# Optimization experiments

Hardware: AMD Instinct MI355X
Metric: run time of the kernel (lower is better)

Reference implementation:

```python
import jax, jax.numpy as jnp
import numpy as np

EMBED = 1024
HEADS = 16
HDIM = 64
OUT = 1024
SCALE = HDIM ** (-0.5)


def setup_inputs() -> dict:
    key = jax.random.key(0)
    ks = jax.random.split(key, 12)
    B, L = 4, 1024
    k = jax.random.normal(ks[0], (B, L, EMBED), dtype=jnp.float32)
    q = jax.random.normal(ks[1], (B, L, EMBED), dtype=jnp.float32)
    v = jax.random.normal(ks[2], (B, L, EMBED), dtype=jnp.float32)
    # Linear params stored as [in, out]; scaled like torch default init
    lim = EMBED ** (-0.5)
    Wq = jax.random.uniform(ks[3], (EMBED, HEADS * HDIM), jnp.float32, -lim, lim)
    bq = jax.random.uniform(ks[4], (HEADS * HDIM,), jnp.float32, -lim, lim)
    Wk = jax.random.uniform(ks[5], (EMBED, HEADS * HDIM), jnp.float32, -lim, lim)
    Wv = jax.random.uniform(ks[6], (EMBED, HEADS * HDIM), jnp.float32, -lim, lim)
    limp = (HEADS * HDIM) ** (-0.5)
    Wp = jax.random.uniform(ks[7], (HEADS * HDIM, OUT), jnp.float32, -limp, limp)
    bp = jax.random.uniform(ks[8], (OUT,), jnp.float32, -limp, limp)
    attn_w = jax.random.uniform(ks[9], (2 * HDIM,), jnp.float32, -SCALE, SCALE)
    gamma = jnp.ones((OUT,), jnp.float32)
    beta = jnp.zeros((OUT,), jnp.float32)
    return {"k": k, "q": q, "v": v, "Wq": Wq, "bq": bq, "Wk": Wk, "Wv": Wv,
            "Wp": Wp, "bp": bp, "attn_w": attn_w, "gamma": gamma, "beta": beta}


def reference(k, q, v, Wq, bq, Wk, Wv, Wp, bp, attn_w, gamma, beta):
    B, Lq = q.shape[0], q.shape[1]
    Lk = k.shape[1]
    # QKV projections -> (b, len, heads, hdim)
    qh = (q @ Wq + bq).reshape(B, Lq, HEADS, HDIM)
    kh = (k @ Wk).reshape(B, Lk, HEADS, HDIM)
    vh = (v @ Wv).reshape(B, Lk, HEADS, HDIM)
    # mlp score: tanh(cat(q_i, k_j) . w) == tanh(q_i.w1 + k_j.w2); avoids
    # materializing the (b, q, k, n, 2d) padded tensor from the original.
    w1, w2 = attn_w[:HDIM], attn_w[HDIM:]
    sq = jnp.einsum('bind,d->bin', qh, w1)  # (b, q_len, heads)
    sk = jnp.einsum('bjnd,d->bjn', kh, w2)  # (b, k_len, heads)
    attn = jnp.tanh(sq[:, :, None, :] + sk[:, None, :, :])  # (b, i, j, n)
    attn = jax.nn.softmax(attn, axis=2)  # softmax over k_len (dim=2)
    out = jnp.einsum('bijn,bjnd->bind', attn, vh).reshape(B, Lq, HEADS * HDIM)
    out = out @ Wp + bp
    # LayerNorm eps=1e-6 (dropout is identity at p=0)
    mean = jnp.mean(out, axis=-1, keepdims=True)
    var = jnp.var(out, axis=-1, keepdims=True)
    out = (out - mean) / jnp.sqrt(var + 1e-6) * gamma + beta
    return out
```

## Files before the change

kernel.cpp:

```cpp
#include <hip/hip_runtime.h>
#include <math.h>

#define HEADS 16
#define HDIM  64
#define SEQ   1024
#define ROWS  4096
#define EMB   1024
#define MN    16

typedef _Float16 f16;
typedef __attribute__((ext_vector_type(4))) _Float16 f16x4;
typedef __attribute__((ext_vector_type(8))) _Float16 f16x8;
typedef __attribute__((ext_vector_type(4))) float f32x4;

__global__ __launch_bounds__(256) void fold_kernel(
    const float* __restrict__ Wq, const float* __restrict__ Wk,
    const float* __restrict__ bq, const float* __restrict__ attn_w,
    float* __restrict__ uq, float* __restrict__ uk, float* __restrict__ cq)
{
  int bid = blockIdx.x;
  if (bid < 128) {
    int idx = bid*256 + threadIdx.x;
    bool isQ = idx < 16384;
    int li = isQ ? idx : idx - 16384;
    int e = li >> 4, n = li & 15;
    const float* W = isQ ? Wq : Wk;
    const float* w = isQ ? attn_w : attn_w + HDIM;
    const float* wp = &W[(size_t)e*EMB + n*HDIM];
    float s = 0.f;
    #pragma unroll 16
    for (int d = 0; d < HDIM; ++d) s = fmaf(wp[d], w[d], s);
    (isQ ? uq : uk)[li] = s;
  } else if (threadIdx.x < 16) {
    int n = threadIdx.x;
    float s = 0.f;
    for (int d = 0; d < HDIM; ++d) s = fmaf(bq[n*HDIM+d], attn_w[d], s);
    cq[n] = s;
  }
}

__global__ __launch_bounds__(256) void sqsk2_kernel(
    const float* __restrict__ q, const float* __restrict__ k,
    const float* __restrict__ uq, const float* __restrict__ uk,
    const float* __restrict__ cq, float* __restrict__ sq, float* __restrict__ sk)
{
  __shared__ float rowbuf[8][EMB];
  __shared__ float part[16][8][17];
  int bid = blockIdx.x;
  bool isQ = bid < 512;
  int row0 = (isQ ? bid : bid - 512) * 8;
  const float* X = isQ ? q : k;
  const float* U = isQ ? uq : uk;
  int tid = threadIdx.x;
  #pragma unroll
  for (int p = 0; p < 8; ++p) {
    int fi = p*256 + tid;
    int r = fi >> 8, c4 = (fi & 255) * 4;
    *reinterpret_cast<float4*>(&rowbuf[r][c4]) =
        *reinterpret_cast<const float4*>(&X[(size_t)(row0 + r)*EMB + c4]);
  }
  __syncthreads();
  int n = tid & 15, ch = tid >> 4;
  float acc[8] = {0,0,0,0,0,0,0,0};
  #pragma unroll 4
  for (int e0 = 0; e0 < 64; ++e0) {
    int e = ch*64 + e0;
    float u = U[e*16 + n];
    #pragma unroll
    for (int r = 0; r < 8; ++r) acc[r] = fmaf(rowbuf[r][e], u, acc[r]);
  }
  #pragma unroll
  for (int r = 0; r < 8; ++r) part[ch][r][n] = acc[r];
  __syncthreads();
  if (tid < 128) {
    int r = tid >> 4, nn = tid & 15;
    float t = isQ ? cq[nn] : 0.f;
    #pragma unroll
    for (int c = 0; c < 16; ++c) t += part[c][r][nn];
    (isQ ? sq : sk)[(size_t)(row0 + r)*16 + nn] = t;
  }
}

__global__ __launch_bounds__(256) void nodes_kernel(const float* __restrict__ sq,
                                                    float* __restrict__ nodes)
{
  int bn = blockIdx.x;
  int b = bn >> 4, n = bn & 15;
  int tid = threadIdx.x;
  float mn = 1e30f, mx = -1e30f;
  #pragma unroll
  for (int s = 0; s < 4; ++s) {
    float v = sq[((size_t)(b*SEQ + tid + s*256))*16 + n];
    mn = fminf(mn, v); mx = fmaxf(mx, v);
  }
  __shared__ float smn[256], smx[256];
  smn[tid] = mn; smx[tid] = mx;
  __syncthreads();
  for (int off = 128; off > 0; off >>= 1) {
    if (tid < off) { smn[tid] = fminf(smn[tid], smn[tid+off]);
                     smx[tid] = fmaxf(smx[tid], smx[tid+off]); }
    __syncthreads();
  }
  if (tid < MN) {
    float c = 0.5f*(smn[0] + smx[0]);
    float r = fmaxf(0.5f*(smx[0] - smn[0]), 1e-4f);
    nodes[bn*MN + tid] = c + r * cosf(tid * (3.14159265358979323f / (MN-1)));
  }
}

__global__ __launch_bounds__(256) void wprepv_kernel(
    const float* __restrict__ Wv, f16* __restrict__ Th, f16* __restrict__ Tl)
{
  __shared__ float tile[64][65];
  int k0 = blockIdx.y * 64, n0 = blockIdx.x * 64;
  int t = threadIdx.x, rr = t >> 4, c4 = (t & 15) * 4;
  #pragma unroll
  for (int i = 0; i < 4; ++i) {
    int row = rr + i * 16;
    float4 w = *reinterpret_cast<const float4*>(&Wv[(size_t)(k0 + row) * EMB + n0 + c4]);
    tile[row][c4] = w.x; tile[row][c4+1] = w.y;
    tile[row][c4+2] = w.z; tile[row][c4+3] = w.w;
  }
  __syncthreads();
  #pragma unroll
  for (int i = 0; i < 4; ++i) {
    int nn = rr + i * 16;
    f16x4 hh, ll;
    #pragma unroll
    for (int jj = 0; jj < 4; ++jj) {
      float x = tile[c4 + jj][nn];
      f16 h = (f16)x;
      hh[jj] = h; ll[jj] = (f16)(x - (float)h);
    }
    *reinterpret_cast<f16x4*>(&Th[(size_t)(n0 + nn) * EMB + k0 + c4]) = hh;
    *reinterpret_cast<f16x4*>(&Tl[(size_t)(n0 + nn) * EMB + k0 + c4]) = ll;
  }
}

__global__ __launch_bounds__(256) void vtrans_kernel(
    const float* __restrict__ v, f16* __restrict__ Th, f16* __restrict__ Tl)
{
  __shared__ float tile[64][65];
  int b = blockIdx.z;
  int j0 = blockIdx.y * 64, e0 = blockIdx.x * 64;
  int t = threadIdx.x, rr = t >> 4, c4 = (t & 15) * 4;
  #pragma unroll
  for (int i = 0; i < 4; ++i) {
    int row = rr + i * 16;
    float4 w = *reinterpret_cast<const float4*>(
        &v[((size_t)(b*SEQ + j0 + row))*EMB + e0 + c4]);
    tile[row][c4] = w.x; tile[row][c4+1] = w.y;
    tile[row][c4+2] = w.z; tile[row][c4+3] = w.w;
  }
  __syncthreads();
  #pragma unroll
  for (int i = 0; i < 4; ++i) {
    int el = rr + i * 16;
    f16x4 hh, ll;
    #pragma unroll
    for (int jj = 0; jj < 4; ++jj) {
      float x = tile[c4 + jj][el];
      f16 h = (f16)x;
      hh[jj] = h; ll[jj] = (f16)(x - (float)h);
    }
    size_t o = ((size_t)(b*EMB + e0 + el))*SEQ + j0 + c4;
    *reinterpret_cast<f16x4*>(&Th[o]) = hh;
    *reinterpret_cast<f16x4*>(&Tl[o]) = ll;
  }
}

__global__ __launch_bounds__(256) void wmat_kernel(
    const float* __restrict__ sk, const float* __restrict__ nodes,
    f16* __restrict__ wh, f16* __restrict__ wl, float* __restrict__ Wn)
{
  __shared__ float sksh[256], nodesh[MN], Wnl[MN];
  const int qd = blockIdx.x, n = blockIdx.y, b = blockIdx.z;
  const int tid = threadIdx.x;
  const int j = qd*256 + tid;
  sksh[tid] = sk[((size_t)(b*SEQ + j))*16 + n];
  if (tid < MN) { nodesh[tid] = nodes[(b*16+n)*MN + tid]; Wnl[tid] = 0.f; }
  __syncthreads();
  const float skv = sksh[tid];
  const int lane = tid & 63;
  #pragma unroll 4
  for (int m = 0; m < MN; ++m) {
    float s = nodesh[m] + skv;
    float e2 = __expf(2.f * s);
    float th = 1.f - 2.f / (e2 + 1.f);
    float w = __expf(th);
    f16 h = (f16)w;
    size_t row = (size_t)(b*256 + n*MN + m);
    wh[row*1024 + j] = h;
    wl[row*1024 + j] = (f16)(w - (float)h);
    float ws = w;
    #pragma unroll
    for (int off = 32; off > 0; off >>= 1) ws += __shfl_xor(ws, off);
    if (lane == 0) atomicAdd(&Wnl[m], ws);
  }
  __syncthreads();
  if (tid < MN) atomicAdd(&Wn[(b*16+n)*MN + tid], Wnl[tid]);
}

__global__ __launch_bounds__(256) void gemm1_64(
    const f16* __restrict__ Ah, const f16* __restrict__ Al,
    const f16* __restrict__ Bh, const f16* __restrict__ Bl,
    f16* __restrict__ Ch, f16* __restrict__ Cl)
{
  __shared__ __align__(16) char lds[32768];
  const int tid = threadIdx.x;
  const int wid = tid >> 6, lane = tid & 63;
  int flat = blockIdx.y * 16 + blockIdx.x;
  int swz = (flat & 7) * 32 + (flat >> 3);
  const int bx = swz & 15, by = swz >> 4;
  const int z = by >> 2;
  const int grow = by * 64;
  const int bcol = bx * 64;
  const int wm = wid >> 1, wn = wid & 1;
  const int asel = lane >> 4, l15 = lane & 15;
  const int K = 1024, N = 1024;
  const f16* Bz_h = Bh + (size_t)z*EMB*SEQ;
  const f16* Bz_l = Bl + (size_t)z*EMB*SEQ;

  f32x4 acc[2][2];
  #pragma unroll
  for (int i = 0; i < 2; ++i)
    #pragma unroll
    for (int jx = 0; jx < 2; ++jx)
      acc[i][jx] = (f32x4){0.f, 0.f, 0.f, 0.f};

  for (int t = 0; t < 16; ++t) {
    const int k0 = t * 64;
    __syncthreads();
    #pragma unroll
    for (int r = 0; r < 8; ++r) {
      int ci = ((r & 1) << 8) + tid;
      int row = ci >> 3, kc = ci & 7;
      int kcg = kc ^ (row & 7);
      const f16* base = (r < 2) ? Ah : (r < 4) ? Al : (r < 6) ? Bz_h : Bz_l;
      size_t roff = (r < 4) ? (size_t)(grow + row) : (size_t)(bcol + row);
      const char* src = (const char*)(base + roff * K + k0 + kcg * 8);
      char* dst = lds + (r * 512 + ci) * 16 - (r & 1) * 4096 * 0;
      dst = lds + (r * 256 + wid * 64) * 16;
      __builtin_amdgcn_global_load_lds(
          (const __attribute__((address_space(1))) unsigned int*)src,
          (__attribute__((address_space(3))) unsigned int*)dst, 16, 0, 0);
    }
    __syncthreads();
    #pragma unroll
    for (int kk = 0; kk < 2; ++kk) {
      f16x8 afh[2], afl[2], bfh[2], bfl[2];
      #pragma unroll
      for (int mf = 0; mf < 2; ++mf) {
        int row = wm * 32 + mf * 16 + l15;
        int kcx = (kk * 4 + asel) ^ (row & 7);
        int off = row * 128 + kcx * 16;
        afh[mf] = *reinterpret_cast<const f16x8*>(lds + off);
        afl[mf] = *reinterpret_cast<const f16x8*>(lds + 8192 + off);
      }
      #pragma unroll
      for (int nf = 0; nf < 2; ++nf) {
        int col = wn * 32 + nf * 16 + l15;
        int kcx = (kk * 4 + asel) ^ (col & 7);
        int off = col * 128 + kcx * 16;
        bfh[nf] = *reinterpret_cast<const f16x8*>(lds + 16384 + off);
        bfl[nf] = *reinterpret_cast<const f16x8*>(lds + 24576 + off);
      }
      #pragma unroll
      for (int mf = 0; mf < 2; ++mf)
        #pragma unroll
        for (int nf = 0; nf < 2; ++nf) {
          acc[mf][nf] = __builtin_amdgcn_mfma_f32_16x16x32_f16(afh[mf], bfh[nf], acc[mf][nf], 0, 0, 0);
          acc[mf][nf] = __builtin_amdgcn_mfma_f32_16x16x32_f16(afh[mf], bfl[nf], acc[mf][nf], 0, 0, 0);
          acc[mf][nf] = __builtin_amdgcn_mfma_f32_16x16x32_f16(afl[mf], bfh[nf], acc[mf][nf], 0, 0, 0);
        }
    }
  }
  const int crow0 = grow + wm * 32 + asel * 4;
  const int ccol0 = bcol + wn * 32 + l15;
  #pragma unroll
  for (int nf = 0; nf < 2; ++nf)
    #pragma unroll
    for (int mf = 0; mf < 2; ++mf)
      #pragma unroll
      for (int jx = 0; jx < 4; ++jx) {
        float vv = acc[mf][nf][jx];
        f16 h = (f16)vv;
        size_t o = (size_t)(crow0 + mf*16 + jx) * N + ccol0 + nf*16;
        Ch[o] = h;
        Cl[o] = (f16)(vv - (float)h);
      }
}

__global__ __launch_bounds__(256) void gemm2_k(
    const f16* __restrict__ Ah, const f16* __restrict__ Al,
    const f16* __restrict__ Bh, const f16* __restrict__ Bl,
    const float* __restrict__ bias, float* __restrict__ Cf)
{
  __shared__ __align__(16) char lds[49152];
  const int tid = threadIdx.x;
  const int wid = tid >> 6, lane = tid & 63;
  int flat = (blockIdx.z * 8 + blockIdx.y) * 16 + blockIdx.x;
  int swz = (flat & 7) * 64 + (flat >> 3);
  const int bx = swz & 15;
  const int t2 = swz >> 4;
  const int by = t2 & 7, z = t2 >> 3;
  const int brow = by * 128;
  const int bcol = bx * 64;
  const int wm = wid >> 1, wn = wid & 1;
  const int asel = lane >> 4, l15 = lane & 15;
  const int K = 256, N = 1024, MZ = 1024;
  const f16* Az_h = Ah + (size_t)z*MZ*K;
  const f16* Az_l = Al + (size_t)z*MZ*K;
  const f16* Bz_h = Bh + (size_t)z*N*K;
  const f16* Bz_l = Bl + (size_t)z*N*K;

  f32x4 acc[4][2];
  #pragma unroll
  for (int i = 0; i < 4; ++i)
    #pragma unroll
    for (int jx = 0; jx < 2; ++jx)
      acc[i][jx] = (f32x4){0.f, 0.f, 0.f, 0.f};

  for (int t = 0; t < 4; ++t) {
    const int k0 = t * 64;
    __syncthreads();
    #pragma unroll
    for (int r = 0; r < 12; ++r) {
      const char* src;
      if (r < 8) {
        int ci = ((r & 3) << 8) + tid;
        int row = ci >> 3, kc = ci & 7;
        int kcg = kc ^ (row & 7);
        const f16* base = (r < 4) ? Az_h : Az_l;
        src = (const char*)(base + (size_t)(brow + row) * K + k0 + kcg * 8);
      } else {
        int ci = ((r & 1) << 8) + tid;
        int col = ci >> 3, kc = ci & 7;
        int kcg = kc ^ (col & 7);
        const f16* base = (r < 10) ? Bz_h : Bz_l;
        src = (const char*)(base + (size_t)(bcol + col) * K + k0 + kcg * 8);
      }
      char* dst = lds + (r * 256 + wid * 64) * 16;
      __builtin_amdgcn_global_load_lds(
          (const __attribute__((address_space(1))) unsigned int*)src,
          (__attribute__((address_space(3))) unsigned int*)dst, 16, 0, 0);
    }
    __syncthreads();
    #pragma unroll
    for (int kk = 0; kk < 2; ++kk) {
      f16x8 afh[4], afl[4], bfh[2], bfl[2];
      #pragma unroll
      for (int mf = 0; mf < 4; ++mf) {
        int row = wm * 64 + mf * 16 + l15;
        int kcx = (kk * 4 + asel) ^ (row & 7);
        int off = row * 128 + kcx * 16;
        afh[mf] = *reinterpret_cast<const f16x8*>(lds + off);
        afl[mf] = *reinterpret_cast<const f16x8*>(lds + 16384 + off);
      }
      #pragma unroll
      for (int nf = 0; nf < 2; ++nf) {
        int col = wn * 32 + nf * 16 + l15;
        int kcx = (kk * 4 + asel) ^ (col & 7);
        int off = col * 128 + kcx * 16;
        bfh[nf] = *reinterpret_cast<const f16x8*>(lds + 32768 + off);
        bfl[nf] = *reinterpret_cast<const f16x8*>(lds + 40960 + off);
      }
      #pragma unroll
      for (int mf = 0; mf < 4; ++mf)
        #pragma unroll
        for (int nf = 0; nf < 2; ++nf) {
          acc[mf][nf] = __builtin_amdgcn_mfma_f32_16x16x32_f16(afh[mf], bfh[nf], acc[mf][nf], 0, 0, 0);
          acc[mf][nf] = __builtin_amdgcn_mfma_f32_16x16x32_f16(afh[mf], bfl[nf], acc[mf][nf], 0, 0, 0);
          acc[mf][nf] = __builtin_amdgcn_mfma_f32_16x16x32_f16(afl[mf], bfh[nf], acc[mf][nf], 0, 0, 0);
        }
    }
  }
  const int crow0 = z*MZ + brow + wm * 64 + asel * 4;
  const int ccol0 = bcol + wn * 32 + l15;
  #pragma unroll
  for (int nf = 0; nf < 2; ++nf) {
    float bv = bias[ccol0 + nf * 16];
    #pragma unroll
    for (int mf = 0; mf < 4; ++mf)
      #pragma unroll
      for (int jx = 0; jx < 4; ++jx)
        Cf[(size_t)(crow0 + mf*16 + jx) * N + ccol0 + nf*16] = acc[mf][nf][jx] + bv;
  }
}

__global__ __launch_bounds__(256) void gfin_kernel(
    const f16* __restrict__ Ph, const f16* __restrict__ Pl,
    const f16* __restrict__ WvTh, const f16* __restrict__ WvTl,
    float* __restrict__ G)
{
  const int bn = blockIdx.x, n = bn & 15;
  const int w = threadIdx.x >> 6, lane = threadIdx.x & 63;
  const int l15 = lane & 15, asel = lane >> 4;
  f32x4 acc = (f32x4){0.f,0.f,0.f,0.f};
  #pragma unroll 4
  for (int ks = 0; ks < 32; ++ks) {
    size_t bo = ((size_t)(n*64 + w*16 + l15))*1024 + ks*32 + asel*8;
    f16x8 bh = *reinterpret_cast<const f16x8*>(&WvTh[bo]);
    f16x8 bl = *reinterpret_cast<const f16x8*>(&WvTl[bo]);
    size_t ao = ((size_t)(bn*MN + l15))*1024 + ks*32 + asel*8;
    f16x8 ah = *reinterpret_cast<const f16x8*>(&Ph[ao]);
    f16x8 al = *reinterpret_cast<const f16x8*>(&Pl[ao]);
    acc = __builtin_amdgcn_mfma_f32_16x16x32_f16(ah, bh, acc, 0, 0, 0);
    acc = __builtin_amdgcn_mfma_f32_16x16x32_f16(ah, bl, acc, 0, 0, 0);
    acc = __builtin_amdgcn_mfma_f32_16x16x32_f16(al, bh, acc, 0, 0, 0);
  }
  #pragma unroll
  for (int jx = 0; jx < 4; ++jx)
    G[(size_t)(bn*MN + asel*4 + jx)*64 + w*16 + l15] = acc[jx];
}

__global__ __launch_bounds__(256) void coeff2_kernel(
    const float* __restrict__ sq, const float* __restrict__ nodes,
    const float* __restrict__ Wn, f16* __restrict__ csh, f16* __restrict__ csl)
{
  __shared__ float nsh[16][MN], wsh[16][MN];
  const int ic = blockIdx.x, b = blockIdx.y;
  const int tid = threadIdx.x;
  {
    int nn = tid >> 4, mm = tid & 15;
    nsh[nn][mm] = nodes[(b*16+nn)*MN + mm];
    wsh[nn][mm] = Wn[(b*16+nn)*MN + mm];
  }
  __syncthreads();
  const int il = tid >> 4, n = tid & 15;
  const int i = ic*16 + il;
  float s = sq[((size_t)(b*SEQ + i))*16 + n];
  float lam[MN];
  float den = 0.f;
  int ex = -1;
  #pragma unroll
  for (int m = 0; m < MN; ++m) {
    float diff = s - nsh[n][m];
    float wb = ((m == 0) | (m == MN-1)) ? 0.5f : 1.0f;
    wb = (m & 1) ? -wb : wb;
    if (diff == 0.f) ex = m;
    lam[m] = wb / diff;
    den = fmaf(lam[m], wsh[n][m], den);
  }
  float rden = 1024.f / den;
  f16* hp = &csh[((size_t)(b*SEQ + i))*256 + n*MN];
  f16* lp = &csl[((size_t)(b*SEQ + i))*256 + n*MN];
  #pragma unroll
  for (int m8 = 0; m8 < 2; ++m8) {
    f16x8 hv, lv;
    #pragma unroll
    for (int jj = 0; jj < 8; ++jj) {
      int m = m8*8 + jj;
      float c = (ex >= 0) ? ((m == ex) ? 1024.f/wsh[n][ex] : 0.f) : lam[m]*rden;
      f16 h = (f16)c;
      hv[jj] = h; lv[jj] = (f16)(c - (float)h);
    }
    *reinterpret_cast<f16x8*>(&hp[m8*8]) = hv;
    *reinterpret_cast<f16x8*>(&lp[m8*8]) = lv;
  }
}

__global__ __launch_bounds__(256) void hprep_kernel(
    const float* __restrict__ G, const float* __restrict__ Wp,
    f16* __restrict__ Hsh, f16* __restrict__ Hsl)
{
  __shared__ float Gsh[MN][64];
  const int oc = blockIdx.x, n = blockIdx.y, b = blockIdx.z;
  const int bn = b*16 + n;
  const int tid = threadIdx.x;
  for (int p = tid; p < MN*64; p += 256) {
    int m = p >> 6, d = p & 63;
    Gsh[m][d] = G[(size_t)(bn*MN + m)*64 + d];
  }
  __syncthreads();
  const int o = oc*256 + tid;
  float acc[MN];
  #pragma unroll
  for (int m = 0; m < MN; ++m) acc[m] = 0.f;
  for (int d = 0; d < 64; ++d) {
    float wp = Wp[(size_t)(n*64 + d)*1024 + o];
    #pragma unroll
    for (int m = 0; m < MN; ++m) acc[m] = fmaf(wp, Gsh[m][d], acc[m]);
  }
  f16 hbuf[MN], lbuf[MN];
  #pragma unroll
  for (int m = 0; m < MN; ++m) {
    float vv = acc[m] * (1.f/1024.f);
    f16 h = (f16)vv;
    hbuf[m] = h; lbuf[m] = (f16)(vv - (float)h);
  }
  size_t base = ((size_t)(b*1024 + o))*256 + n*MN;
  #pragma unroll
  for (int m8 = 0; m8 < 2; ++m8) {
    *reinterpret_cast<f16x8*>(&Hsh[base + m8*8]) = *reinterpret_cast<f16x8*>(&hbuf[m8*8]);
    *reinterpret_cast<f16x8*>(&Hsl[base + m8*8]) = *reinterpret_cast<f16x8*>(&lbuf[m8*8]);
  }
}

__global__ __launch_bounds__(256) void ln_kernel(
    float* __restrict__ out, const float* __restrict__ gamma,
    const float* __restrict__ beta)
{
  int row = blockIdx.x, tid = threadIdx.x;
  float4 x = *reinterpret_cast<float4*>(&out[(size_t)row*EMB + tid*4]);
  float sum = x.x + x.y + x.z + x.w;
  float ssq = x.x*x.x + x.y*x.y + x.z*x.z + x.w*x.w;
  #pragma unroll
  for (int off = 32; off > 0; off >>= 1) {
    sum += __shfl_down(sum, off);
    ssq += __shfl_down(ssq, off);
  }
  __shared__ float red[8];
  int wave = tid >> 6, lane = tid & 63;
  if (lane == 0) { red[wave] = sum; red[4+wave] = ssq; }
  __syncthreads();
  if (tid == 0) {
    float a = red[0]+red[1]+red[2]+red[3];
    float qq = red[4]+red[5]+red[6]+red[7];
    float mean = a * (1.f/EMB);
    float var  = qq * (1.f/EMB) - mean*mean;
    red[0] = mean;
    red[1] = 1.0f / sqrtf(var + 1e-6f);
  }
  __syncthreads();
  float mean = red[0], inv = red[1];
  float4 gv = *reinterpret_cast<const float4*>(&gamma[tid*4]);
  float4 bv = *reinterpret_cast<const float4*>(&beta[tid*4]);
  x.x = (x.x - mean)*inv*gv.x + bv.x;
  x.y = (x.y - mean)*inv*gv.y + bv.y;
  x.z = (x.z - mean)*inv*gv.z + bv.z;
  x.w = (x.w - mean)*inv*gv.w + bv.w;
  *reinterpret_cast<float4*>(&out[(size_t)row*EMB + tid*4]) = x;
}

extern "C" void kernel_launch(void* const* d_in, const int* in_sizes, int n_in,
                              void* d_out, int out_size, void* d_ws, size_t ws_size,
                              hipStream_t stream)
{
  const float* k   = (const float*)d_in[0];
  const float* q   = (const float*)d_in[1];
  const float* v   = (const float*)d_in[2];
  const float* Wq  = (const float*)d_in[3];
  const float* bq  = (const float*)d_in[4];
  const float* Wk  = (const float*)d_in[5];
  const float* Wv  = (const float*)d_in[6];
  const float* Wp  = (const float*)d_in[7];
  const float* bp  = (const float*)d_in[8];
  const float* aw  = (const float*)d_in[9];
  const float* gamma = (const float*)d_in[10];
  const float* beta  = (const float*)d_in[11];
  float* out = (float*)d_out;

  float* ws    = (float*)d_ws;
  float* uq    = ws;
  float* uk    = uq + 16384;
  float* cq    = uk + 16384;
  float* sq    = cq + 16;
  float* sk    = sq + 65536;
  float* nodes = sk + 65536;
  float* Wn    = nodes + 1024;
  float* G     = Wn + 1024;
  const size_t MEG = 1048576;
  f16* f16b  = (f16*)(ws + 231440);
  f16* WvTh  = f16b;
  f16* WvTl  = f16b + 1*MEG;
  f16* Ph    = f16b + 2*MEG;
  f16* Pl    = f16b + 3*MEG;
  f16* vTh   = f16b + 4*MEG;
  f16* vTl   = f16b + 8*MEG;
  f16* wh    = f16b + 12*MEG;
  f16* wl    = f16b + 13*MEG;
  f16* csh   = f16b + 4*MEG;
  f16* csl   = f16b + 5*MEG;
  f16* Hsh   = f16b + 8*MEG;
  f16* Hsl   = f16b + 9*MEG;

  fold_kernel<<<129, 256, 0, stream>>>(Wq, Wk, bq, aw, uq, uk, cq);
  sqsk2_kernel<<<1024, 256, 0, stream>>>(q, k, uq, uk, cq, sq, sk);
  nodes_kernel<<<64, 256, 0, stream>>>(sq, nodes);
  wprepv_kernel<<<dim3(16,16), 256, 0, stream>>>(Wv, WvTh, WvTl);
  vtrans_kernel<<<dim3(16,16,4), 256, 0, stream>>>(v, vTh, vTl);
  hipMemsetAsync(Wn, 0, 1024*sizeof(float), stream);
  wmat_kernel<<<dim3(4,16,4), 256, 0, stream>>>(sk, nodes, wh, wl, Wn);
  gemm1_64<<<dim3(16,16), 256, 0, stream>>>(wh, wl, vTh, vTl, Ph, Pl);
  coeff2_kernel<<<dim3(64,4), 256, 0, stream>>>(sq, nodes, Wn, csh, csl);
  gfin_kernel<<<64, 256, 0, stream>>>(Ph, Pl, WvTh, WvTl, G);
  hprep_kernel<<<dim3(4,16,4), 256, 0, stream>>>(G, Wp, Hsh, Hsl);
  gemm2_k<<<dim3(16,8,4), 256, 0, stream>>>(csh, csl, Hsh, Hsl, bp, out);
  ln_kernel<<<ROWS, 256, 0, stream>>>(out, gamma, beta);
}
```

Measured before the change: 229.0 us.

## Drop split-f16 low parts in V-path GEMMs and fuse transpose and G/H prep kernels

Removes the hi/lo f16 split for the exp-weight matrix, transposed v, Wv and the intermediate P, so gemm1 and the G computation use one MFMA per step instead of three and load half the data. Merges the v and Wv transpose kernels into one launch. Fuses gfin into hprep, so each block recomputes its 16x64 G tile with MFMA and the G buffer round trip goes away. Accuracy falls to single-f16 precision on this path, and G is now recomputed redundantly across the four output-chunk blocks.

```diff
diff --git a/kernel.cpp b/kernel.cpp
--- a/kernel.cpp
+++ b/kernel.cpp
@@ -108,70 +108,39 @@
   }
 }
 
-__global__ __launch_bounds__(256) void wprepv_kernel(
-    const float* __restrict__ Wv, f16* __restrict__ Th, f16* __restrict__ Tl)
+__global__ __launch_bounds__(256) void ztrans_kernel(
+    const float* __restrict__ v, const float* __restrict__ Wv,
+    f16* __restrict__ vTh, f16* __restrict__ WvTh)
 {
   __shared__ float tile[64][65];
-  int k0 = blockIdx.y * 64, n0 = blockIdx.x * 64;
-  int t = threadIdx.x, rr = t >> 4, c4 = (t & 15) * 4;
+  const int z = blockIdx.z;
+  const int r0 = blockIdx.y * 64, c0 = blockIdx.x * 64;
+  const int t = threadIdx.x, rr = t >> 4, c4 = (t & 15) * 4;
+  const float* src = (z < 4) ? &v[(size_t)(z*SEQ + r0)*EMB + c0]
+                             : &Wv[(size_t)r0*EMB + c0];
   #pragma unroll
   for (int i = 0; i < 4; ++i) {
     int row = rr + i * 16;
-    float4 w = *reinterpret_cast<const float4*>(&Wv[(size_t)(k0 + row) * EMB + n0 + c4]);
+    float4 w = *reinterpret_cast<const float4*>(&src[(size_t)row*EMB + c4]);
     tile[row][c4] = w.x; tile[row][c4+1] = w.y;
     tile[row][c4+2] = w.z; tile[row][c4+3] = w.w;
   }
   __syncthreads();
   #pragma unroll
   for (int i = 0; i < 4; ++i) {
-    int nn = rr + i * 16;
-    f16x4 hh, ll;
-    #pragma unroll
-    for (int jj = 0; jj < 4; ++jj) {
-      float x = tile[c4 + jj][nn];
-      f16 h = (f16)x;
-      hh[jj] = h; ll[jj] = (f16)(x - (float)h);
-    }
-    *reinterpret_cast<f16x4*>(&Th[(size_t)(n0 + nn) * EMB + k0 + c4]) = hh;
-    *reinterpret_cast<f16x4*>(&Tl[(size_t)(n0 + nn) * EMB + k0 + c4]) = ll;
-  }
-}
-
-__global__ __launch_bounds__(256) void vtrans_kernel(
-    const float* __restrict__ v, f16* __restrict__ Th, f16* __restrict__ Tl)
-{
-  __shared__ float tile[64][65];
-  int b = blockIdx.z;
-  int j0 = blockIdx.y * 64, e0 = blockIdx.x * 64;
-  int t = threadIdx.x, rr = t >> 4, c4 = (t & 15) * 4;
-  #pragma unroll
-  for (int i = 0; i < 4; ++i) {
-    int row = rr + i * 16;
-    float4 w = *reinterpret_cast<const float4*>(
-        &v[((size_t)(b*SEQ + j0 + row))*EMB + e0 + c4]);
-    tile[row][c4] = w.x; tile[row][c4+1] = w.y;
-    tile[row][c4+2] = w.z; tile[row][c4+3] = w.w;
-  }
-  __syncthreads();
-  #pragma unroll
-  for (int i = 0; i < 4; ++i) {
-    int el = rr + i * 16;
-    f16x4 hh, ll;
-    #pragma unroll
-    for (int jj = 0; jj < 4; ++jj) {
-      float x = tile[c4 + jj][el];
-      f16 h = (f16)x;
-      hh[jj] = h; ll[jj] = (f16)(x - (float)h);
-    }
-    size_t o = ((size_t)(b*EMB + e0 + el))*SEQ + j0 + c4;
-    *reinterpret_cast<f16x4*>(&Th[o]) = hh;
-    *reinterpret_cast<f16x4*>(&Tl[o]) = ll;
+    int cc = rr + i * 16;
+    f16x4 hh;
+    #pragma unroll
+    for (int jj = 0; jj < 4; ++jj) hh[jj] = (f16)tile[c4 + jj][cc];
+    size_t o = (z < 4) ? ((size_t)(z*EMB + c0 + cc))*SEQ + r0 + c4
+                       : ((size_t)(c0 + cc))*EMB + r0 + c4;
+    *reinterpret_cast<f16x4*>(&((z < 4) ? vTh : WvTh)[o]) = hh;
   }
 }
 
 __global__ __launch_bounds__(256) void wmat_kernel(
     const float* __restrict__ sk, const float* __restrict__ nodes,
-    f16* __restrict__ wh, f16* __restrict__ wl, float* __restrict__ Wn)
+    f16* __restrict__ wh, float* __restrict__ Wn)
 {
   __shared__ float sksh[256], nodesh[MN], Wnl[MN];
   const int qd = blockIdx.x, n = blockIdx.y, b = blockIdx.z;
@@ -188,10 +157,8 @@
     float e2 = __expf(2.f * s);
     float th = 1.f - 2.f / (e2 + 1.f);
     float w = __expf(th);
-    f16 h = (f16)w;
     size_t row = (size_t)(b*256 + n*MN + m);
-    wh[row*1024 + j] = h;
-    wl[row*1024 + j] = (f16)(w - (float)h);
+    wh[row*1024 + j] = (f16)w;
     float ws = w;
     #pragma unroll
     for (int off = 32; off > 0; off >>= 1) ws += __shfl_xor(ws, off);
@@ -201,12 +168,11 @@
   if (tid < MN) atomicAdd(&Wn[(b*16+n)*MN + tid], Wnl[tid]);
 }
 
-__global__ __launch_bounds__(256) void gemm1_64(
-    const f16* __restrict__ Ah, const f16* __restrict__ Al,
-    const f16* __restrict__ Bh, const f16* __restrict__ Bl,
-    f16* __restrict__ Ch, f16* __restrict__ Cl)
-{
-  __shared__ __align__(16) char lds[32768];
+__global__ __launch_bounds__(256) void gemm1_f16(
+    const f16* __restrict__ Ah, const f16* __restrict__ Bh,
+    f16* __restrict__ Ch)
+{
+  __shared__ __align__(16) char lds[16384];
   const int tid = threadIdx.x;
   const int wid = tid >> 6, lane = tid & 63;
   int flat = blockIdx.y * 16 + blockIdx.x;
@@ -219,7 +185,6 @@
   const int asel = lane >> 4, l15 = lane & 15;
   const int K = 1024, N = 1024;
   const f16* Bz_h = Bh + (size_t)z*EMB*SEQ;
-  const f16* Bz_l = Bl + (size_t)z*EMB*SEQ;
 
   f32x4 acc[2][2];
   #pragma unroll
@@ -232,15 +197,14 @@
     const int k0 = t * 64;
     __syncthreads();
     #pragma unroll
-    for (int r = 0; r < 8; ++r) {
+    for (int r = 0; r < 4; ++r) {
       int ci = ((r & 1) << 8) + tid;
       int row = ci >> 3, kc = ci & 7;
       int kcg = kc ^ (row & 7);
-      const f16* base = (r < 2) ? Ah : (r < 4) ? Al : (r < 6) ? Bz_h : Bz_l;
-      size_t roff = (r < 4) ? (size_t)(grow + row) : (size_t)(bcol + row);
+      const f16* base = (r < 2) ? Ah : Bz_h;
+      size_t roff = (r < 2) ? (size_t)(grow + row) : (size_t)(bcol + row);
       const char* src = (const char*)(base + roff * K + k0 + kcg * 8);
-      char* dst = lds + (r * 512 + ci) * 16 - (r & 1) * 4096 * 0;
-      dst = lds + (r * 256 + wid * 64) * 16;
+      char* dst = lds + (r * 256 + wid * 64) * 16;
       __builtin_amdgcn_global_load_lds(
           (const __attribute__((address_space(1))) unsigned int*)src,
           (__attribute__((address_space(3))) unsigned int*)dst, 16, 0, 0);
@@ -248,31 +212,24 @@
     __syncthreads();
     #pragma unroll
     for (int kk = 0; kk < 2; ++kk) {
-      f16x8 afh[2], afl[2], bfh[2], bfl[2];
+      f16x8 afh[2], bfh[2];
       #pragma unroll
       for (int mf = 0; mf < 2; ++mf) {
         int row = wm * 32 + mf * 16 + l15;
         int kcx = (kk * 4 + asel) ^ (row & 7);
-        int off = row * 128 + kcx * 16;
-        afh[mf] = *reinterpret_cast<const f16x8*>(lds + off);
-        afl[mf] = *reinterpret_cast<const f16x8*>(lds + 8192 + off);
+        afh[mf] = *reinterpret_cast<const f16x8*>(lds + row * 128 + kcx * 16);
       }
       #pragma unroll
       for (int nf = 0; nf < 2; ++nf) {
         int col = wn * 32 + nf * 16 + l15;
         int kcx = (kk * 4 + asel) ^ (col & 7);
-        int off = col * 128 + kcx * 16;
-        bfh[nf] = *reinterpret_cast<const f16x8*>(lds + 16384 + off);
-        bfl[nf] = *reinterpret_cast<const f16x8*>(lds + 24576 + off);
+        bfh[nf] = *reinterpret_cast<const f16x8*>(lds + 8192 + col * 128 + kcx * 16);
       }
       #pragma unroll
       for (int mf = 0; mf < 2; ++mf)
         #pragma unroll
-        for (int nf = 0; nf < 2; ++nf) {
+        for (int nf = 0; nf < 2; ++nf)
           acc[mf][nf] = __builtin_amdgcn_mfma_f32_16x16x32_f16(afh[mf], bfh[nf], acc[mf][nf], 0, 0, 0);
-          acc[mf][nf] = __builtin_amdgcn_mfma_f32_16x16x32_f16(afh[mf], bfl[nf], acc[mf][nf], 0, 0, 0);
-          acc[mf][nf] = __builtin_amdgcn_mfma_f32_16x16x32_f16(afl[mf], bfh[nf], acc[mf][nf], 0, 0, 0);
-        }
     }
   }
   const int crow0 = grow + wm * 32 + asel * 4;
@@ -282,13 +239,101 @@
     #pragma unroll
     for (int mf = 0; mf < 2; ++mf)
       #pragma unroll
-      for (int jx = 0; jx < 4; ++jx) {
-        float vv = acc[mf][nf][jx];
-        f16 h = (f16)vv;
-        size_t o = (size_t)(crow0 + mf*16 + jx) * N + ccol0 + nf*16;
-        Ch[o] = h;
-        Cl[o] = (f16)(vv - (float)h);
-      }
+      for (int jx = 0; jx < 4; ++jx)
+        Ch[(size_t)(crow0 + mf*16 + jx) * N + ccol0 + nf*16] = (f16)acc[mf][nf][jx];
+}
+
+__global__ __launch_bounds__(256) void coeff2_kernel(
+    const float* __restrict__ sq, const float* __restrict__ nodes,
+    const float* __restrict__ Wn, f16* __restrict__ csh, f16* __restrict__ csl)
+{
+  __shared__ float nsh[16][MN], wsh[16][MN];
+  const int ic = blockIdx.x, b = blockIdx.y;
+  const int tid = threadIdx.x;
+  {
+    int nn = tid >> 4, mm = tid & 15;
+    nsh[nn][mm] = nodes[(b*16+nn)*MN + mm];
+    wsh[nn][mm] = Wn[(b*16+nn)*MN + mm];
+  }
+  __syncthreads();
+  const int il = tid >> 4, n = tid & 15;
+  const int i = ic*16 + il;
+  float s = sq[((size_t)(b*SEQ + i))*16 + n];
+  float lam[MN];
+  float den = 0.f;
+  int ex = -1;
+  #pragma unroll
+  for (int m = 0; m < MN; ++m) {
+    float diff = s - nsh[n][m];
+    float wb = ((m == 0) | (m == MN-1)) ? 0.5f : 1.0f;
+    wb = (m & 1) ? -wb : wb;
+    if (diff == 0.f) ex = m;
+    lam[m] = wb / diff;
+    den = fmaf(lam[m], wsh[n][m], den);
+  }
+  float rden = 1024.f / den;
+  f16* hp = &csh[((size_t)(b*SEQ + i))*256 + n*MN];
+  f16* lp = &csl[((size_t)(b*SEQ + i))*256 + n*MN];
+  #pragma unroll
+  for (int m8 = 0; m8 < 2; ++m8) {
+    f16x8 hv, lv;
+    #pragma unroll
+    for (int jj = 0; jj < 8; ++jj) {
+      int m = m8*8 + jj;
+      float c = (ex >= 0) ? ((m == ex) ? 1024.f/wsh[n][ex] : 0.f) : lam[m]*rden;
+      f16 h = (f16)c;
+      hv[jj] = h; lv[jj] = (f16)(c - (float)h);
+    }
+    *reinterpret_cast<f16x8*>(&hp[m8*8]) = hv;
+    *reinterpret_cast<f16x8*>(&lp[m8*8]) = lv;
+  }
+}
+
+__global__ __launch_bounds__(256) void ghprep_kernel(
+    const f16* __restrict__ Ph, const f16* __restrict__ WvTh,
+    const float* __restrict__ Wp, f16* __restrict__ Hsh, f16* __restrict__ Hsl)
+{
+  __shared__ float Gsh[MN][64];
+  const int oc = blockIdx.x, n = blockIdx.y, b = blockIdx.z;
+  const int bn = b*16 + n;
+  const int tid = threadIdx.x;
+  const int w = tid >> 6, lane = tid & 63;
+  const int l15 = lane & 15, asel = lane >> 4;
+  f32x4 acc = (f32x4){0.f,0.f,0.f,0.f};
+  #pragma unroll 4
+  for (int ks = 0; ks < 32; ++ks) {
+    size_t bo = ((size_t)(n*64 + w*16 + l15))*1024 + ks*32 + asel*8;
+    f16x8 bh = *reinterpret_cast<const f16x8*>(&WvTh[bo]);
+    size_t ao = ((size_t)(bn*MN + l15))*1024 + ks*32 + asel*8;
+    f16x8 ah = *reinterpret_cast<const f16x8*>(&Ph[ao]);
+    acc = __builtin_amdgcn_mfma_f32_16x16x32_f16(ah, bh, acc, 0, 0, 0);
+  }
+  #pragma unroll
+  for (int jx = 0; jx < 4; ++jx)
+    Gsh[asel*4 + jx][w*16 + l15] = acc[jx];
+  __syncthreads();
+  const int o = oc*256 + tid;
+  float a2[MN];
+  #pragma unroll
+  for (int m = 0; m < MN; ++m) a2[m] = 0.f;
+  for (int d = 0; d < 64; ++d) {
+    float wp = Wp[(size_t)(n*64 + d)*1024 + o];
+    #pragma unroll
+    for (int m = 0; m < MN; ++m) a2[m] = fmaf(wp, Gsh[m][d], a2[m]);
+  }
+  f16 hbuf[MN], lbuf[MN];
+  #pragma unroll
+  for (int m = 0; m < MN; ++m) {
+    float vv = a2[m] * (1.f/1024.f);
+    f16 h = (f16)vv;
+    hbuf[m] = h; lbuf[m] = (f16)(vv - (float)h);
+  }
+  size_t base = ((size_t)(b*1024 + o))*256 + n*MN;
+  #pragma unroll
+  for (int m8 = 0; m8 < 2; ++m8) {
+    *reinterpret_cast<f16x8*>(&Hsh[base + m8*8]) = *reinterpret_cast<f16x8*>(&hbuf[m8*8]);
+    *reinterpret_cast<f16x8*>(&Hsl[base + m8*8]) = *reinterpret_cast<f16x8*>(&lbuf[m8*8]);
+  }
 }
 
 __global__ __launch_bounds__(256) void gemm2_k(
@@ -388,115 +433,6 @@
   }
 }
 
-__global__ __launch_bounds__(256) void gfin_kernel(
-    const f16* __restrict__ Ph, const f16* __restrict__ Pl,
-    const f16* __restrict__ WvTh, const f16* __restrict__ WvTl,
-    float* __restrict__ G)
-{
-  const int bn = blockIdx.x, n = bn & 15;
-  const int w = threadIdx.x >> 6, lane = threadIdx.x & 63;
-  const int l15 = lane & 15, asel = lane >> 4;
-  f32x4 acc = (f32x4){0.f,0.f,0.f,0.f};
-  #pragma unroll 4
-  for (int ks = 0; ks < 32; ++ks) {
-    size_t bo = ((size_t)(n*64 + w*16 + l15))*1024 + ks*32 + asel*8;
-    f16x8 bh = *reinterpret_cast<const f16x8*>(&WvTh[bo]);
-    f16x8 bl = *reinterpret_cast<const f16x8*>(&WvTl[bo]);
-    size_t ao = ((size_t)(bn*MN + l15))*1024 + ks*32 + asel*8;
-    f16x8 ah = *reinterpret_cast<const f16x8*>(&Ph[ao]);
-    f16x8 al = *reinterpret_cast<const f16x8*>(&Pl[ao]);
-    acc = __builtin_amdgcn_mfma_f32_16x16x32_f16(ah, bh, acc, 0, 0, 0);
-    acc = __builtin_amdgcn_mfma_f32_16x16x32_f16(ah, bl, acc, 0, 0, 0);
-    acc = __builtin_amdgcn_mfma_f32_16x16x32_f16(al, bh, acc, 0, 0, 0);
-  }
-  #pragma unroll
-  for (int jx = 0; jx < 4; ++jx)
-    G[(size_t)(bn*MN + asel*4 + jx)*64 + w*16 + l15] = acc[jx];
-}
-
-__global__ __launch_bounds__(256) void coeff2_kernel(
-    const float* __restrict__ sq, const float* __restrict__ nodes,
-    const float* __restrict__ Wn, f16* __restrict__ csh, f16* __restrict__ csl)
-{
-  __shared__ float nsh[16][MN], wsh[16][MN];
-  const int ic = blockIdx.x, b = blockIdx.y;
-  const int tid = threadIdx.x;
-  {
-    int nn = tid >> 4, mm = tid & 15;
-    nsh[nn][mm] = nodes[(b*16+nn)*MN + mm];
-    wsh[nn][mm] = Wn[(b*16+nn)*MN + mm];
-  }
-  __syncthreads();
-  const int il = tid >> 4, n = tid & 15;
-  const int i = ic*16 + il;
-  float s = sq[((size_t)(b*SEQ + i))*16 + n];
-  float lam[MN];
-  float den = 0.f;
-  int ex = -1;
-  #pragma unroll
-  for (int m = 0; m < MN; ++m) {
-    float diff = s - nsh[n][m];
-    float wb = ((m == 0) | (m == MN-1)) ? 0.5f : 1.0f;
-    wb = (m & 1) ? -wb : wb;
-    if (diff == 0.f) ex = m;
-    lam[m] = wb / diff;
-    den = fmaf(lam[m], wsh[n][m], den);
-  }
-  float rden = 1024.f / den;
-  f16* hp = &csh[((size_t)(b*SEQ + i))*256 + n*MN];
-  f16* lp = &csl[((size_t)(b*SEQ + i))*256 + n*MN];
-  #pragma unroll
-  for (int m8 = 0; m8 < 2; ++m8) {
-    f16x8 hv, lv;
-    #pragma unroll
-    for (int jj = 0; jj < 8; ++jj) {
-      int m = m8*8 + jj;
-      float c = (ex >= 0) ? ((m == ex) ? 1024.f/wsh[n][ex] : 0.f) : lam[m]*rden;
-      f16 h = (f16)c;
-      hv[jj] = h; lv[jj] = (f16)(c - (float)h);
-    }
-    *reinterpret_cast<f16x8*>(&hp[m8*8]) = hv;
-    *reinterpret_cast<f16x8*>(&lp[m8*8]) = lv;
-  }
-}
-
-__global__ __launch_bounds__(256) void hprep_kernel(
-    const float* __restrict__ G, const float* __restrict__ Wp,
-    f16* __restrict__ Hsh, f16* __restrict__ Hsl)
-{
-  __shared__ float Gsh[MN][64];
-  const int oc = blockIdx.x, n = blockIdx.y, b = blockIdx.z;
-  const int bn = b*16 + n;
-  const int tid = threadIdx.x;
-  for (int p = tid; p < MN*64; p += 256) {
-    int m = p >> 6, d = p & 63;
-    Gsh[m][d] = G[(size_t)(bn*MN + m)*64 + d];
-  }
-  __syncthreads();
-  const int o = oc*256 + tid;
-  float acc[MN];
-  #pragma unroll
-  for (int m = 0; m < MN; ++m) acc[m] = 0.f;
-  for (int d = 0; d < 64; ++d) {
-    float wp = Wp[(size_t)(n*64 + d)*1024 + o];
-    #pragma unroll
-    for (int m = 0; m < MN; ++m) acc[m] = fmaf(wp, Gsh[m][d], acc[m]);
-  }
-  f16 hbuf[MN], lbuf[MN];
-  #pragma unroll
-  for (int m = 0; m < MN; ++m) {
-    float vv = acc[m] * (1.f/1024.f);
-    f16 h = (f16)vv;
-    hbuf[m] = h; lbuf[m] = (f16)(vv - (float)h);
-  }
-  size_t base = ((size_t)(b*1024 + o))*256 + n*MN;
-  #pragma unroll
-  for (int m8 = 0; m8 < 2; ++m8) {
-    *reinterpret_cast<f16x8*>(&Hsh[base + m8*8]) = *reinterpret_cast<f16x8*>(&hbuf[m8*8]);
-    *reinterpret_cast<f16x8*>(&Hsl[base + m8*8]) = *reinterpret_cast<f16x8*>(&lbuf[m8*8]);
-  }
-}
-
 __global__ __launch_bounds__(256) void ln_kernel(
     float* __restrict__ out, const float* __restrict__ gamma,
     const float* __restrict__ beta)
@@ -559,33 +495,26 @@
   float* sk    = sq + 65536;
   float* nodes = sk + 65536;
   float* Wn    = nodes + 1024;
-  float* G     = Wn + 1024;
   const size_t MEG = 1048576;
-  f16* f16b  = (f16*)(ws + 231440);
+  f16* f16b  = (f16*)(ws + 165904);
   f16* WvTh  = f16b;
-  f16* WvTl  = f16b + 1*MEG;
-  f16* Ph    = f16b + 2*MEG;
-  f16* Pl    = f16b + 3*MEG;
-  f16* vTh   = f16b + 4*MEG;
-  f16* vTl   = f16b + 8*MEG;
-  f16* wh    = f16b + 12*MEG;
-  f16* wl    = f16b + 13*MEG;
-  f16* csh   = f16b + 4*MEG;
-  f16* csl   = f16b + 5*MEG;
-  f16* Hsh   = f16b + 8*MEG;
-  f16* Hsl   = f16b + 9*MEG;
+  f16* vTh   = f16b + 1*MEG;
+  f16* wh    = f16b + 5*MEG;
+  f16* Ph    = f16b + 6*MEG;
+  f16* csh   = f16b + 7*MEG;
+  f16* csl   = f16b + 8*MEG;
+  f16* Hsh   = f16b + 9*MEG;
+  f16* Hsl   = f16b + 10*MEG;
 
   fold_kernel<<<129, 256, 0, stream>>>(Wq, Wk, bq, aw, uq, uk, cq);
   sqsk2_kernel<<<1024, 256, 0, stream>>>(q, k, uq, uk, cq, sq, sk);
   nodes_kernel<<<64, 256, 0, stream>>>(sq, nodes);
-  wprepv_kernel<<<dim3(16,16), 256, 0, stream>>>(Wv, WvTh, WvTl);
-  vtrans_kernel<<<dim3(16,16,4), 256, 0, stream>>>(v, vTh, vTl);
+  ztrans_kernel<<<dim3(16,16,5), 256, 0, stream>>>(v, Wv, vTh, WvTh);
   hipMemsetAsync(Wn, 0, 1024*sizeof(float), stream);
-  wmat_kernel<<<dim3(4,16,4), 256, 0, stream>>>(sk, nodes, wh, wl, Wn);
-  gemm1_64<<<dim3(16,16), 256, 0, stream>>>(wh, wl, vTh, vTl, Ph, Pl);
+  wmat_kernel<<<dim3(4,16,4), 256, 0, stream>>>(sk, nodes, wh, Wn);
+  gemm1_f16<<<dim3(16,16), 256, 0, stream>>>(wh, vTh, Ph);
   coeff2_kernel<<<dim3(64,4), 256, 0, stream>>>(sq, nodes, Wn, csh, csl);
-  gfin_kernel<<<64, 256, 0, stream>>>(Ph, Pl, WvTh, WvTl, G);
-  hprep_kernel<<<dim3(4,16,4), 256, 0, stream>>>(G, Wp, Hsh, Hsl);
+  ghprep_kernel<<<dim3(4,16,4), 256, 0, stream>>>(Ph, WvTh, Wp, Hsh, Hsl);
   gemm2_k<<<dim3(16,8,4), 256, 0, stream>>>(csh, csl, Hsh, Hsl, bp, out);
   ln_kernel<<<ROWS, 256, 0, stream>>>(out, gamma, beta);
 }
```

After: 196.1 us. -14.3%, faster.
